# Optimization experiments

Measured on AMD Instinct MI355X. Metric: run time of the kernel, lower is better.

Reference implementation:

```python
import jax, jax.numpy as jnp
import numpy as np

N_NODES = 50000
N_EDGES = 800000
EMBED = 128
HEADS = 8
HEAD_DIM = EMBED // HEADS  # 16
HIDDEN = 512
EPS = 1e-5
SLOPE = 0.2  # DGL GATConv default negative_slope


def setup_inputs() -> dict:
    key = jax.random.key(0)
    ks = jax.random.split(key, 16)
    s = 0.05
    return {
        "x": jax.random.normal(ks[0], (N_NODES, EMBED), dtype=jnp.float32),
        "src": jax.random.randint(ks[1], (N_EDGES,), 0, N_NODES),
        "dst": jax.random.randint(ks[2], (N_EDGES,), 0, N_NODES),
        # GATConv params: fc weight stored as [in, out] (i.e. torch weight transposed)
        "W": jax.random.normal(ks[3], (EMBED, HEADS * HEAD_DIM), dtype=jnp.float32) * s,
        "attn_l": jax.random.normal(ks[4], (HEADS, HEAD_DIM), dtype=jnp.float32) * s,
        "attn_r": jax.random.normal(ks[5], (HEADS, HEAD_DIM), dtype=jnp.float32) * s,
        "gat_bias": jnp.zeros((EMBED,), dtype=jnp.float32),
        # BatchNorm1d affine params (training-mode batch stats used in math)
        "gamma1": jnp.ones((EMBED,), dtype=jnp.float32),
        "beta1": jnp.zeros((EMBED,), dtype=jnp.float32),
        "gamma2": jnp.ones((EMBED,), dtype=jnp.float32),
        "beta2": jnp.zeros((EMBED,), dtype=jnp.float32),
        # FFN weights stored as [in, out]
        "W1": jax.random.normal(ks[6], (EMBED, HIDDEN), dtype=jnp.float32) * s,
        "b1": jnp.zeros((HIDDEN,), dtype=jnp.float32),
        "W2": jax.random.normal(ks[7], (HIDDEN, EMBED), dtype=jnp.float32) * s,
        "b2": jnp.zeros((EMBED,), dtype=jnp.float32),
    }


def _batchnorm(y, gamma, beta):
    mu = jnp.mean(y, axis=0)
    var = jnp.var(y, axis=0)  # biased variance, as torch BN uses for normalization
    return gamma * (y - mu) * jax.lax.rsqrt(var + EPS) + beta


def reference(x, src, dst, W, attn_l, attn_r, gat_bias,
              gamma1, beta1, gamma2, beta2, W1, b1, W2, b2):
    N = x.shape[0]
    # ---- GATConv ----
    feat = (x @ W).reshape(N, HEADS, HEAD_DIM)              # [N,H,D]
    el = jnp.sum(feat * attn_l, axis=-1)                    # [N,H]
    er = jnp.sum(feat * attn_r, axis=-1)                    # [N,H]
    e = jax.nn.leaky_relu(el[src] + er[dst], SLOPE)         # [E,H]
    # segment softmax over incoming edges of each dst node
    m = jax.ops.segment_max(e, dst, num_segments=N)         # [N,H] (-inf for empty)
    ex = jnp.exp(e - m[dst])                                # [E,H]
    denom = jax.ops.segment_sum(ex, dst, num_segments=N)    # [N,H]
    a = ex / denom[dst]                                     # [E,H]
    msg = feat[src] * a[:, :, None]                         # [E,H,D]
    rst = jax.ops.segment_sum(msg, dst, num_segments=N)     # [N,H,D]
    rst = rst + gat_bias.reshape(HEADS, HEAD_DIM)
    h = x + rst.reshape(N, EMBED)                           # skip connection
    # ---- FFN block: BN -> skip(MLP) -> BN ----
    h = _batchnorm(h, gamma1, beta1)
    y = jax.nn.relu(h @ W1 + b1) @ W2 + b2
    h = _batchnorm(h + y, gamma2, beta2)
    return h
```

## Files before the change

kernel.cpp:

```cpp
#include <hip/hip_runtime.h>

#define NCH 128
#define NH  8
#define HID 512
#define SLOPE 0.2f
#define BN_EPS 1e-5f
#define LDP 136
#define NPW 4

typedef __attribute__((ext_vector_type(8))) short short8;
typedef __attribute__((ext_vector_type(4))) float floatx4;

__device__ inline unsigned short f2bf(float f) {
  unsigned u = __float_as_uint(f);
  u += 0x7fffu + ((u >> 16) & 1u);
  return (unsigned short)(u >> 16);
}
__device__ inline float bflo(unsigned u) { return __uint_as_float(u << 16); }
__device__ inline float bfhi(unsigned u) { return __uint_as_float(u & 0xffff0000u); }

__global__ void prep_all(const float* __restrict__ W, unsigned short* __restrict__ WT,
                         const float* __restrict__ W1, unsigned short* __restrict__ w1f,
                         const float* __restrict__ W2, unsigned short* __restrict__ w2f,
                         float* __restrict__ stats, int* __restrict__ cnt, int N) {
  int b = blockIdx.x, tid = threadIdx.x;
  if (b < 64) {
    int i = b * 256 + tid;
    int n = i >> 7, k = i & 127;
    WT[i] = f2bf(W[k * NCH + n]);
  } else if (b < 320) {
    int i = (b - 64) * 256 + tid;
    int ntile = i >> 11, kk = (i >> 9) & 3, lane = (i >> 3) & 63, j = i & 7;
    int k = kk * 32 + (lane >> 4) * 8 + j;
    int n = ntile * 16 + (lane & 15);
    w1f[i] = f2bf(W1[k * HID + n]);
  } else if (b < 576) {
    int i = (b - 320) * 256 + tid;
    int ch = i >> 14, nt = (i >> 11) & 7, kk = (i >> 9) & 3, lane = (i >> 3) & 63, j = i & 7;
    int k = ch * 128 + kk * 32 + (lane >> 4) * 8 + j;
    int n = nt * 16 + (lane & 15);
    w2f[i] = f2bf(W2[k * NCH + n]);
  } else if (b < 596) {
    int i = (b - 576) * 256 + tid;
    ((float4*)stats)[i] = make_float4(0.f, 0.f, 0.f, 0.f);
  } else {
    int i = (b - 596) * 256 + tid;
    int n4 = (N + 3) >> 2;
    if (i < n4) ((int4*)cnt)[i] = make_int4(0, 0, 0, 0);
  }
}

__global__ __launch_bounds__(256) void feat_mfma(const float* __restrict__ x,
                                                 const unsigned short* __restrict__ WT,
                                                 const float* __restrict__ attn_l,
                                                 const float* __restrict__ attn_r,
                                                 unsigned short* __restrict__ featb,
                                                 float* __restrict__ el, float* __restrict__ er,
                                                 int N) {
  __shared__ unsigned short rowX[64 * LDP];
  __shared__ unsigned short wt[128 * LDP];
  __shared__ float alr[256];
  int tid = threadIdx.x;
  int r0 = blockIdx.x * 64;
  int lane = tid & 63, wid = tid >> 6;
  int quad = lane >> 4, lc = lane & 15;
  int mrow = (wid & 1) * 32;
  int chalf = (wid >> 1) * 64;

  alr[tid] = (tid < 128) ? attn_l[tid] : attn_r[tid - 128];
  {
    int n = tid >> 1, kg = (tid & 1) * 64;
    const uint4* g = (const uint4*)(WT + n * NCH + kg);
    uint4* l = (uint4*)&wt[n * LDP + kg];
    for (int i = 0; i < 8; i++) l[i] = g[i];
  }
  {
    int r = tid >> 2, kg = (tid & 3) * 32;
    int gr = r0 + r;
    unsigned short tmp[32];
    if (gr < N) {
      const float4* gp = (const float4*)(x + (size_t)gr * NCH + kg);
      for (int i = 0; i < 8; i++) {
        float4 v = gp[i];
        tmp[i * 4 + 0] = f2bf(v.x); tmp[i * 4 + 1] = f2bf(v.y);
        tmp[i * 4 + 2] = f2bf(v.z); tmp[i * 4 + 3] = f2bf(v.w);
      }
    } else {
      for (int i = 0; i < 32; i++) tmp[i] = 0;
    }
    uint4* l = (uint4*)&rowX[r * LDP + kg];
    const uint4* s = (const uint4*)tmp;
    for (int i = 0; i < 4; i++) l[i] = s[i];
  }
  __syncthreads();

  floatx4 acc[2][4];
  for (int rt = 0; rt < 2; rt++) for (int tt = 0; tt < 4; tt++) acc[rt][tt] = (floatx4)(0.f);
  for (int kk = 0; kk < 4; kk++) {
    short8 a0 = *(const short8*)&rowX[(mrow + lc) * LDP + kk * 32 + quad * 8];
    short8 a1 = *(const short8*)&rowX[(mrow + 16 + lc) * LDP + kk * 32 + quad * 8];
    for (int tt = 0; tt < 4; tt++) {
      short8 b = *(const short8*)&wt[(chalf + tt * 16 + lc) * LDP + kk * 32 + quad * 8];
      acc[0][tt] = __builtin_amdgcn_mfma_f32_16x16x32_bf16(a0, b, acc[0][tt], 0, 0, 0);
      acc[1][tt] = __builtin_amdgcn_mfma_f32_16x16x32_bf16(a1, b, acc[1][tt], 0, 0, 0);
    }
  }
  __syncthreads();
  for (int rt = 0; rt < 2; rt++)
    for (int tt = 0; tt < 4; tt++)
      for (int r = 0; r < 4; r++)
        rowX[(mrow + rt * 16 + quad * 4 + r) * LDP + chalf + tt * 16 + lc] = f2bf(acc[rt][tt][r]);
  __syncthreads();
  {
    int r = tid >> 2, kg = (tid & 3) * 32;
    int gr = r0 + r;
    if (gr < N) {
      uint4* gp = (uint4*)(featb + (size_t)gr * NCH + kg);
      const uint4* l = (const uint4*)&rowX[r * LDP + kg];
      for (int i = 0; i < 4; i++) gp[i] = l[i];
    }
  }
  for (int p = tid; p < 512; p += 256) {
    int row = p >> 3, h = p & 7;
    int gr = r0 + row;
    if (gr < N) {
      const unsigned* rp = (const unsigned*)&rowX[row * LDP + h * 16];
      float sl = 0.f, sr = 0.f;
      for (int q = 0; q < 8; q++) {
        unsigned u = rp[q];
        float lo = bflo(u), hi = bfhi(u);
        int c = h * 16 + 2 * q;
        sl += lo * alr[c] + hi * alr[c + 1];
        sr += lo * alr[128 + c] + hi * alr[128 + c + 1];
      }
      el[gr * NH + h] = sl;
      er[gr * NH + h] = sr;
    }
  }
}

__global__ void edge_hist(const int* __restrict__ dst, int* __restrict__ cnt, int E) {
  int i = blockIdx.x * 256 + threadIdx.x;
  if (i < E) atomicAdd(&cnt[dst[i]], 1);
}

__global__ void scan_part(const int* __restrict__ cnt, int* __restrict__ off,
                          int* __restrict__ bsum, int N) {
  __shared__ int sh[256];
  int t = threadIdx.x, i = blockIdx.x * 256 + t;
  int v = (i < N) ? cnt[i] : 0;
  sh[t] = v; __syncthreads();
  for (int d = 1; d < 256; d <<= 1) {
    int u = (t >= d) ? sh[t - d] : 0;
    __syncthreads();
    sh[t] += u;
    __syncthreads();
  }
  if (i < N) off[i] = sh[t] - v;
  if (t == 255) bsum[blockIdx.x] = sh[255];
}

__global__ void scan_top(int* __restrict__ bsum, int nb) {
  __shared__ int sh[256];
  int t = threadIdx.x;
  int v = (t < nb) ? bsum[t] : 0;
  sh[t] = v; __syncthreads();
  for (int d = 1; d < 256; d <<= 1) {
    int u = (t >= d) ? sh[t - d] : 0;
    __syncthreads();
    sh[t] += u;
    __syncthreads();
  }
  if (t < nb) bsum[t] = sh[t] - v;
}

__global__ void scan_add(int* __restrict__ off, const int* __restrict__ bsum,
                         int* __restrict__ cursor, int N) {
  int i = blockIdx.x * 256 + threadIdx.x;
  if (i < N) {
    int v = off[i] + bsum[blockIdx.x];
    off[i] = v;
    cursor[i] = v;
  }
}

__global__ void edge_scatter(const int* __restrict__ src, const int* __restrict__ dst,
                             int* __restrict__ cursor, int* __restrict__ ssrc, int E) {
  int i = blockIdx.x * 256 + threadIdx.x;
  if (i < E) {
    int p = atomicAdd(&cursor[dst[i]], 1);
    ssrc[p] = src[i];
  }
}

__global__ __launch_bounds__(256) void gat_gather6(const int* __restrict__ ssrc,
                                                   const int* __restrict__ off,
                                                   const int* __restrict__ cnt,
                                                   const float* __restrict__ el,
                                                   const float* __restrict__ er,
                                                   const unsigned short* __restrict__ featb,
                                                   const float* __restrict__ x,
                                                   const float* __restrict__ gatb,
                                                   float* __restrict__ hbuf,
                                                   float* __restrict__ stats, int N) {
  __shared__ float ps[4][128], pq[4][128];
  int tid = threadIdx.x;
  int lane = tid & 63, w = tid >> 6;
  int hme = lane >> 3;
  int c0 = 2 * lane;
  float gb0 = gatb[c0], gb1 = gatb[c0 + 1];
  float s0 = 0.f, s1 = 0.f, q0 = 0.f, q1 = 0.f;
  int base = blockIdx.x * (4 * NPW) + w * NPW;
  for (int j = 0; j < NPW; j++) {
    int node = base + j;
    if (node >= N) break;
    node = __builtin_amdgcn_readfirstlane(node);
    float erh = er[node * NH + hme];
    int beg = __builtin_amdgcn_readfirstlane(off[node]);
    int num = __builtin_amdgcn_readfirstlane(cnt[node]);
    const int* sp = ssrc + beg;
    float acc0 = 0.f, acc1 = 0.f, den = 0.f;
    int i = 0;
    for (; i + 8 <= num; i += 8) {
      int n0 = __builtin_amdgcn_readfirstlane(sp[i + 0]);
      int n1 = __builtin_amdgcn_readfirstlane(sp[i + 1]);
      int n2 = __builtin_amdgcn_readfirstlane(sp[i + 2]);
      int n3 = __builtin_amdgcn_readfirstlane(sp[i + 3]);
      int n4 = __builtin_amdgcn_readfirstlane(sp[i + 4]);
      int n5 = __builtin_amdgcn_readfirstlane(sp[i + 5]);
      int n6 = __builtin_amdgcn_readfirstlane(sp[i + 6]);
      int n7 = __builtin_amdgcn_readfirstlane(sp[i + 7]);
      unsigned f0 = ((const unsigned*)(featb + (size_t)n0 * NCH))[lane];
      unsigned f1 = ((const unsigned*)(featb + (size_t)n1 * NCH))[lane];
      unsigned f2 = ((const unsigned*)(featb + (size_t)n2 * NCH))[lane];
      unsigned f3 = ((const unsigned*)(featb + (size_t)n3 * NCH))[lane];
      unsigned f4 = ((const unsigned*)(featb + (size_t)n4 * NCH))[lane];
      unsigned f5 = ((const unsigned*)(featb + (size_t)n5 * NCH))[lane];
      unsigned f6 = ((const unsigned*)(featb + (size_t)n6 * NCH))[lane];
      unsigned f7 = ((const unsigned*)(featb + (size_t)n7 * NCH))[lane];
      float e0 = el[n0 * NH + hme] + erh, e1 = el[n1 * NH + hme] + erh;
      float e2 = el[n2 * NH + hme] + erh, e3 = el[n3 * NH + hme] + erh;
      float e4 = el[n4 * NH + hme] + erh, e5 = el[n5 * NH + hme] + erh;
      float e6 = el[n6 * NH + hme] + erh, e7 = el[n7 * NH + hme] + erh;
      e0 = e0 > 0.f ? e0 : SLOPE * e0;  e1 = e1 > 0.f ? e1 : SLOPE * e1;
      e2 = e2 > 0.f ? e2 : SLOPE * e2;  e3 = e3 > 0.f ? e3 : SLOPE * e3;
      e4 = e4 > 0.f ? e4 : SLOPE * e4;  e5 = e5 > 0.f ? e5 : SLOPE * e5;
      e6 = e6 > 0.f ? e6 : SLOPE * e6;  e7 = e7 > 0.f ? e7 : SLOPE * e7;
      float w0 = __expf(e0), w1 = __expf(e1), w2 = __expf(e2), w3 = __expf(e3);
      float w4 = __expf(e4), w5 = __expf(e5), w6 = __expf(e6), w7 = __expf(e7);
      acc0 += w0 * bflo(f0) + w1 * bflo(f1) + w2 * bflo(f2) + w3 * bflo(f3)
            + w4 * bflo(f4) + w5 * bflo(f5) + w6 * bflo(f6) + w7 * bflo(f7);
      acc1 += w0 * bfhi(f0) + w1 * bfhi(f1) + w2 * bfhi(f2) + w3 * bfhi(f3)
            + w4 * bfhi(f4) + w5 * bfhi(f5) + w6 * bfhi(f6) + w7 * bfhi(f7);
      den  += w0 + w1 + w2 + w3 + w4 + w5 + w6 + w7;
    }
    for (; i + 4 <= num; i += 4) {
      int n0 = __builtin_amdgcn_readfirstlane(sp[i + 0]);
      int n1 = __builtin_amdgcn_readfirstlane(sp[i + 1]);
      int n2 = __builtin_amdgcn_readfirstlane(sp[i + 2]);
      int n3 = __builtin_amdgcn_readfirstlane(sp[i + 3]);
      unsigned f0 = ((const unsigned*)(featb + (size_t)n0 * NCH))[lane];
      unsigned f1 = ((const unsigned*)(featb + (size_t)n1 * NCH))[lane];
      unsigned f2 = ((const unsigned*)(featb + (size_t)n2 * NCH))[lane];
      unsigned f3 = ((const unsigned*)(featb + (size_t)n3 * NCH))[lane];
      float e0 = el[n0 * NH + hme] + erh, e1 = el[n1 * NH + hme] + erh;
      float e2 = el[n2 * NH + hme] + erh, e3 = el[n3 * NH + hme] + erh;
      e0 = e0 > 0.f ? e0 : SLOPE * e0;  e1 = e1 > 0.f ? e1 : SLOPE * e1;
      e2 = e2 > 0.f ? e2 : SLOPE * e2;  e3 = e3 > 0.f ? e3 : SLOPE * e3;
      float w0 = __expf(e0), w1 = __expf(e1), w2 = __expf(e2), w3 = __expf(e3);
      acc0 += w0 * bflo(f0) + w1 * bflo(f1) + w2 * bflo(f2) + w3 * bflo(f3);
      acc1 += w0 * bfhi(f0) + w1 * bfhi(f1) + w2 * bfhi(f2) + w3 * bfhi(f3);
      den  += w0 + w1 + w2 + w3;
    }
    for (; i < num; i++) {
      int s = __builtin_amdgcn_readfirstlane(sp[i]);
      unsigned f = ((const unsigned*)(featb + (size_t)s * NCH))[lane];
      float e = el[s * NH + hme] + erh;
      e = e > 0.f ? e : SLOPE * e;
      float wv = __expf(e);
      acc0 += wv * bflo(f); acc1 += wv * bfhi(f); den += wv;
    }
    float inv = den > 0.f ? 1.f / den : 0.f;
    float2 xv = *(const float2*)(x + (size_t)node * NCH + c0);
    float h0 = xv.x + acc0 * inv + gb0;
    float h1 = xv.y + acc1 * inv + gb1;
    *(float2*)(hbuf + (size_t)node * NCH + c0) = make_float2(h0, h1);
    s0 += h0; s1 += h1; q0 += h0 * h0; q1 += h1 * h1;
  }
  ps[w][c0] = s0; ps[w][c0 + 1] = s1;
  pq[w][c0] = q0; pq[w][c0 + 1] = q1;
  __syncthreads();
  if (tid < 128) {
    float ss = ps[0][tid] + ps[1][tid] + ps[2][tid] + ps[3][tid];
    float qq = pq[0][tid] + pq[1][tid] + pq[2][tid] + pq[3][tid];
    int rep = blockIdx.x & 3;
    atomicAdd(&stats[rep * 2048 + tid * 16], ss);
    atomicAdd(&stats[8192 + rep * 2048 + tid * 16], qq);
  }
}

__global__ void stats_finalize(const float* __restrict__ stats, float* __restrict__ mu,
                               float* __restrict__ rs, int n, int so_sum, int so_sq, int nrep) {
  int c = threadIdx.x;
  if (c < 128) {
    float s = 0.f, sq = 0.f;
    for (int r = 0; r < nrep; r++) {
      s  += stats[so_sum + r * 2048 + c * 16];
      sq += stats[so_sq  + r * 2048 + c * 16];
    }
    float m = s / (float)n;
    float v = sq / (float)n - m * m;
    mu[c] = m;
    rs[c] = rsqrtf(v + BN_EPS);
  }
}

__global__ __launch_bounds__(512, 4) void ffn_mfma2(const float* __restrict__ hbuf,
                                                    const float* __restrict__ mu1, const float* __restrict__ rs1,
                                                    const float* __restrict__ g1, const float* __restrict__ be1,
                                                    const unsigned short* __restrict__ w1f,
                                                    const unsigned short* __restrict__ w2f,
                                                    const float* __restrict__ b1, const float* __restrict__ b2,
                                                    float* __restrict__ t, float* __restrict__ stats, int N) {
  __shared__ unsigned short w1t[16384];
  __shared__ unsigned short w2t[16384];
  __shared__ unsigned short scr[8][512];
  __shared__ float b1L[512];
  __shared__ float psc[128], psh[128], b2L[128], csum[128], csq[128];
  int tid = threadIdx.x;
  int lane = tid & 63, wid = tid >> 6;
  int quad = lane >> 4, lc = lane & 15;
  int r0 = blockIdx.x * 128;

  b1L[tid] = b1[tid];
  if (tid < 128) {
    float s = g1[tid] * rs1[tid];
    psc[tid] = s;
    psh[tid] = be1[tid] - s * mu1[tid];
    b2L[tid] = b2[tid];
    csum[tid] = 0.f; csq[tid] = 0.f;
  }

  int arow = r0 + wid * 16 + lc;
  float4 av[4][2];
  for (int kk = 0; kk < 4; kk++) {
    if (arow < N) {
      const float4* p = (const float4*)(hbuf + (size_t)arow * NCH + kk * 32 + quad * 8);
      av[kk][0] = p[0]; av[kk][1] = p[1];
    } else {
      av[kk][0] = make_float4(0.f, 0.f, 0.f, 0.f);
      av[kk][1] = make_float4(0.f, 0.f, 0.f, 0.f);
    }
  }
  __syncthreads();

  short8 rowA[4];
  for (int kk = 0; kk < 4; kk++) {
    int c = kk * 32 + quad * 8;
    float4 s0 = *(float4*)&psc[c], s1 = *(float4*)&psc[c + 4];
    float4 h0 = *(float4*)&psh[c], h1 = *(float4*)&psh[c + 4];
    short8 r;
    r[0] = (short)f2bf(av[kk][0].x * s0.x + h0.x);
    r[1] = (short)f2bf(av[kk][0].y * s0.y + h0.y);
    r[2] = (short)f2bf(av[kk][0].z * s0.z + h0.z);
    r[3] = (short)f2bf(av[kk][0].w * s0.w + h0.w);
    r[4] = (short)f2bf(av[kk][1].x * s1.x + h1.x);
    r[5] = (short)f2bf(av[kk][1].y * s1.y + h1.y);
    r[6] = (short)f2bf(av[kk][1].z * s1.z + h1.z);
    r[7] = (short)f2bf(av[kk][1].w * s1.w + h1.w);
    rowA[kk] = r;
  }

  floatx4 acc2[8];
  for (int nt = 0; nt < 8; nt++) acc2[nt] = (floatx4)(0.f);

  for (int ch = 0; ch < 4; ch++) {
    __syncthreads();
    {
      const uint4* g1p = (const uint4*)(w1f + ch * 16384);
      const uint4* g2p = (const uint4*)(w2f + ch * 16384);
      uint4* l1 = (uint4*)w1t;
      uint4* l2 = (uint4*)w2t;
      for (int r = 0; r < 4; r++) {
        l1[tid + r * 512] = g1p[tid + r * 512];
        l2[tid + r * 512] = g2p[tid + r * 512];
      }
    }
    __syncthreads();

    for (int kk = 0; kk < 4; kk++) {
      floatx4 d0 = (floatx4)(0.f), d1 = (floatx4)(0.f);
      int t0 = 2 * kk, t1 = 2 * kk + 1;
      for (int kp = 0; kp < 4; kp++) {
        short8 a0 = *(const short8*)&w1t[(t0 * 4 + kp) * 512 + lane * 8];
        short8 a1 = *(const short8*)&w1t[(t1 * 4 + kp) * 512 + lane * 8];
        d0 = __builtin_amdgcn_mfma_f32_16x16x32_bf16(a0, rowA[kp], d0, 0, 0, 0);
        d1 = __builtin_amdgcn_mfma_f32_16x16x32_bf16(a1, rowA[kp], d1, 0, 0, 0);
      }
      {
        int bi0 = ch * 128 + t0 * 16 + 4 * quad;
        float4 bv0 = *(float4*)&b1L[bi0];
        float4 bv1 = *(float4*)&b1L[bi0 + 16];
        float v0, v1, v2, v3;
        unsigned lo, hi;
        int sidx;
        v0 = fmaxf(d0[0] + bv0.x, 0.f); v1 = fmaxf(d0[1] + bv0.y, 0.f);
        v2 = fmaxf(d0[2] + bv0.z, 0.f); v3 = fmaxf(d0[3] + bv0.w, 0.f);
        lo = (unsigned)f2bf(v0) | ((unsigned)f2bf(v1) << 16);
        hi = (unsigned)f2bf(v2) | ((unsigned)f2bf(v3) << 16);
        sidx = ((quad >> 1) * 16 + lc) * 8 + 4 * (quad & 1);
        *(uint2*)&scr[wid][sidx] = make_uint2(lo, hi);
        v0 = fmaxf(d1[0] + bv1.x, 0.f); v1 = fmaxf(d1[1] + bv1.y, 0.f);
        v2 = fmaxf(d1[2] + bv1.z, 0.f); v3 = fmaxf(d1[3] + bv1.w, 0.f);
        lo = (unsigned)f2bf(v0) | ((unsigned)f2bf(v1) << 16);
        hi = (unsigned)f2bf(v2) | ((unsigned)f2bf(v3) << 16);
        sidx = ((2 + (quad >> 1)) * 16 + lc) * 8 + 4 * (quad & 1);
        *(uint2*)&scr[wid][sidx] = make_uint2(lo, hi);
      }
      short8 a2 = *(const short8*)&scr[wid][lane * 8];
      for (int nt = 0; nt < 8; nt++) {
        short8 bfr = *(const short8*)&w2t[(nt * 4 + kk) * 512 + lane * 8];
        acc2[nt] = __builtin_amdgcn_mfma_f32_16x16x32_bf16(a2, bfr, acc2[nt], 0, 0, 0);
      }
    }
  }

  for (int nt = 0; nt < 8; nt++) {
    int col = nt * 16 + lc;
    float sc = psc[col], sh = psh[col], b2v = b2L[col];
    float s = 0.f, q = 0.f;
    for (int reg = 0; reg < 4; reg++) {
      int grow = r0 + wid * 16 + quad * 4 + reg;
      if (grow < N) {
        float hb = hbuf[(size_t)grow * NCH + col];
        float base = __uint_as_float(((unsigned)f2bf(sc * hb + sh)) << 16);
        float tv = base + acc2[nt][reg] + b2v;
        t[(size_t)grow * NCH + col] = tv;
        s += tv; q += tv * tv;
      }
    }
    s += __shfl_xor(s, 16); s += __shfl_xor(s, 32);
    q += __shfl_xor(q, 16); q += __shfl_xor(q, 32);
    if (quad == 0) { atomicAdd(&csum[col], s); atomicAdd(&csq[col], q); }
  }
  __syncthreads();
  if (tid < 128) {
    atomicAdd(&stats[16384 + tid * 16], csum[tid]);
    atomicAdd(&stats[18432 + tid * 16], csq[tid]);
  }
}

__global__ void bn2_apply(const float* __restrict__ t,
                          const float* __restrict__ g, const float* __restrict__ b,
                          const float* __restrict__ mu, const float* __restrict__ rs,
                          float* __restrict__ out, int total) {
  int i = blockIdx.x * blockDim.x + threadIdx.x;
  if (i >= total) return;
  int c = i & 127;
  out[i] = g[c] * (t[i] - mu[c]) * rs[c] + b[c];
}

extern "C" void kernel_launch(void* const* d_in, const int* in_sizes, int n_in,
                              void* d_out, int out_size, void* d_ws, size_t ws_size,
                              hipStream_t stream) {
  const float* x       = (const float*)d_in[0];
  const int*   src     = (const int*)d_in[1];
  const int*   dst     = (const int*)d_in[2];
  const float* W       = (const float*)d_in[3];
  const float* attn_l  = (const float*)d_in[4];
  const float* attn_r  = (const float*)d_in[5];
  const float* gatb    = (const float*)d_in[6];
  const float* gamma1  = (const float*)d_in[7];
  const float* beta1   = (const float*)d_in[8];
  const float* gamma2  = (const float*)d_in[9];
  const float* beta2   = (const float*)d_in[10];
  const float* W1      = (const float*)d_in[11];
  const float* b1      = (const float*)d_in[12];
  const float* W2      = (const float*)d_in[13];
  const float* b2      = (const float*)d_in[14];
  float* out = (float*)d_out;

  const int N = in_sizes[0] / NCH;
  const int E = in_sizes[1];
  const int nb = (N + 255) / 256;

  float* hbuf  = (float*)d_ws;
  float* t     = hbuf + (size_t)N * NCH;
  float* el    = t + (size_t)N * NCH;
  float* er    = el + (size_t)N * NH;
  float* stats = er + (size_t)N * NH;
  float* mus   = stats + 20480;
  unsigned short* featb = (unsigned short*)(mus + 512);
  unsigned short* WT    = featb + (size_t)N * NCH;
  unsigned short* w1f   = WT + NCH * NCH;
  unsigned short* w2f   = w1f + HID * NCH;
  int* cnt    = (int*)(w2f + HID * NCH);
  int* off    = cnt + N;
  int* cursor = off + N;
  int* bsum   = cursor + N;
  int* ssrc   = bsum + 256;

  const int cb = (((N + 3) / 4) + 255) / 256;
  prep_all<<<596 + cb, 256, 0, stream>>>(W, WT, W1, w1f, W2, w2f, stats, cnt, N);

  feat_mfma<<<(N + 63) / 64, 256, 0, stream>>>(x, WT, attn_l, attn_r, featb, el, er, N);

  edge_hist<<<(E + 255) / 256, 256, 0, stream>>>(dst, cnt, E);
  scan_part<<<nb, 256, 0, stream>>>(cnt, off, bsum, N);
  scan_top<<<1, 256, 0, stream>>>(bsum, nb);
  scan_add<<<nb, 256, 0, stream>>>(off, bsum, cursor, N);
  edge_scatter<<<(E + 255) / 256, 256, 0, stream>>>(src, dst, cursor, ssrc, E);

  gat_gather6<<<(N + 4 * NPW - 1) / (4 * NPW), 256, 0, stream>>>(ssrc, off, cnt, el, er, featb,
                                                                 x, gatb, hbuf, stats, N);
  stats_finalize<<<1, 128, 0, stream>>>(stats, mus, mus + 128, N, 0, 8192, 4);

  ffn_mfma2<<<(N + 127) / 128, 512, 0, stream>>>(hbuf, mus, mus + 128, gamma1, beta1,
                                                 w1f, w2f, b1, b2, t, stats, N);
  stats_finalize<<<1, 128, 0, stream>>>(stats, mus + 256, mus + 384, N, 16384, 18432, 1);

  bn2_apply<<<(N * NCH + 255) / 256, 256, 0, stream>>>(t, gamma2, beta2,
                                                       mus + 256, mus + 384, out, N * NCH);
}
```

Baseline: 324.6 us.

## Fuse launches: merge hist into feat kernel, fold scans and stats finalize into consumers

Merges the edge histogram into the feature MFMA kernel as extra blocks, merges the top-level scan into the scan-add kernel (each block recomputes the block prefix), and folds both BN stats finalizations into the FFN and BN2 apply kernels. BN2 apply is also vectorised to float4. This removes four kernel launches and their serialisation gaps, at the cost of redundant per-block stats and scan recomputation. The histogram atomics now run concurrently with the MFMA blocks.

```diff
diff --git a/kernel.cpp b/kernel.cpp
--- a/kernel.cpp
+++ b/kernel.cpp
@@ -50,16 +50,23 @@
   }
 }
 
-__global__ __launch_bounds__(256) void feat_mfma(const float* __restrict__ x,
+__global__ __launch_bounds__(256) void feat_hist(const float* __restrict__ x,
                                                  const unsigned short* __restrict__ WT,
                                                  const float* __restrict__ attn_l,
                                                  const float* __restrict__ attn_r,
                                                  unsigned short* __restrict__ featb,
                                                  float* __restrict__ el, float* __restrict__ er,
-                                                 int N) {
+                                                 int N,
+                                                 const int* __restrict__ dst, int* __restrict__ cnt,
+                                                 int E, int FB) {
   __shared__ unsigned short rowX[64 * LDP];
   __shared__ unsigned short wt[128 * LDP];
   __shared__ float alr[256];
+  if (blockIdx.x >= FB) {
+    int i = (blockIdx.x - FB) * 256 + threadIdx.x;
+    if (i < E) atomicAdd(&cnt[dst[i]], 1);
+    return;
+  }
   int tid = threadIdx.x;
   int r0 = blockIdx.x * 64;
   int lane = tid & 63, wid = tid >> 6;
@@ -139,11 +146,6 @@
   }
 }
 
-__global__ void edge_hist(const int* __restrict__ dst, int* __restrict__ cnt, int E) {
-  int i = blockIdx.x * 256 + threadIdx.x;
-  if (i < E) atomicAdd(&cnt[dst[i]], 1);
-}
-
 __global__ void scan_part(const int* __restrict__ cnt, int* __restrict__ off,
                           int* __restrict__ bsum, int N) {
   __shared__ int sh[256];
@@ -160,7 +162,8 @@
   if (t == 255) bsum[blockIdx.x] = sh[255];
 }
 
-__global__ void scan_top(int* __restrict__ bsum, int nb) {
+__global__ void scan_add2(int* __restrict__ off, const int* __restrict__ bsum,
+                          int* __restrict__ cursor, int N, int nb) {
   __shared__ int sh[256];
   int t = threadIdx.x;
   int v = (t < nb) ? bsum[t] : 0;
@@ -171,16 +174,12 @@
     sh[t] += u;
     __syncthreads();
   }
-  if (t < nb) bsum[t] = sh[t] - v;
-}
-
-__global__ void scan_add(int* __restrict__ off, const int* __restrict__ bsum,
-                         int* __restrict__ cursor, int N) {
-  int i = blockIdx.x * 256 + threadIdx.x;
+  int pref = (blockIdx.x > 0) ? sh[blockIdx.x - 1] : 0;
+  int i = blockIdx.x * 256 + t;
   if (i < N) {
-    int v = off[i] + bsum[blockIdx.x];
-    off[i] = v;
-    cursor[i] = v;
+    int w = off[i] + pref;
+    off[i] = w;
+    cursor[i] = w;
   }
 }
 
@@ -299,24 +298,7 @@
   }
 }
 
-__global__ void stats_finalize(const float* __restrict__ stats, float* __restrict__ mu,
-                               float* __restrict__ rs, int n, int so_sum, int so_sq, int nrep) {
-  int c = threadIdx.x;
-  if (c < 128) {
-    float s = 0.f, sq = 0.f;
-    for (int r = 0; r < nrep; r++) {
-      s  += stats[so_sum + r * 2048 + c * 16];
-      sq += stats[so_sq  + r * 2048 + c * 16];
-    }
-    float m = s / (float)n;
-    float v = sq / (float)n - m * m;
-    mu[c] = m;
-    rs[c] = rsqrtf(v + BN_EPS);
-  }
-}
-
 __global__ __launch_bounds__(512, 4) void ffn_mfma2(const float* __restrict__ hbuf,
-                                                    const float* __restrict__ mu1, const float* __restrict__ rs1,
                                                     const float* __restrict__ g1, const float* __restrict__ be1,
                                                     const unsigned short* __restrict__ w1f,
                                                     const unsigned short* __restrict__ w2f,
@@ -334,9 +316,17 @@
 
   b1L[tid] = b1[tid];
   if (tid < 128) {
-    float s = g1[tid] * rs1[tid];
-    psc[tid] = s;
-    psh[tid] = be1[tid] - s * mu1[tid];
+    float s = 0.f, sq = 0.f;
+    for (int r = 0; r < 4; r++) {
+      s  += stats[r * 2048 + tid * 16];
+      sq += stats[8192 + r * 2048 + tid * 16];
+    }
+    float m = s / (float)N;
+    float v = sq / (float)N - m * m;
+    float rsv = rsqrtf(v + BN_EPS);
+    float scv = g1[tid] * rsv;
+    psc[tid] = scv;
+    psh[tid] = be1[tid] - scv * m;
     b2L[tid] = b2[tid];
     csum[tid] = 0.f; csq[tid] = 0.f;
   }
@@ -450,14 +440,34 @@
   }
 }
 
-__global__ void bn2_apply(const float* __restrict__ t,
-                          const float* __restrict__ g, const float* __restrict__ b,
-                          const float* __restrict__ mu, const float* __restrict__ rs,
-                          float* __restrict__ out, int total) {
-  int i = blockIdx.x * blockDim.x + threadIdx.x;
-  if (i >= total) return;
-  int c = i & 127;
-  out[i] = g[c] * (t[i] - mu[c]) * rs[c] + b[c];
+__global__ __launch_bounds__(256) void bn2_apply2(const float* __restrict__ t,
+                                                  const float* __restrict__ g, const float* __restrict__ b,
+                                                  const float* __restrict__ stats,
+                                                  float* __restrict__ out, int N) {
+  __shared__ float scs[128], shs[128];
+  int tid = threadIdx.x;
+  if (tid < 128) {
+    float s = stats[16384 + tid * 16], sq = stats[18432 + tid * 16];
+    float m = s / (float)N;
+    float v = sq / (float)N - m * m;
+    float rsv = rsqrtf(v + BN_EPS);
+    float gg = g[tid] * rsv;
+    scs[tid] = gg;
+    shs[tid] = b[tid] - gg * m;
+  }
+  __syncthreads();
+  int i = blockIdx.x * 256 + tid;
+  int tot4 = N * 32;
+  if (i < tot4) {
+    float4 v = ((const float4*)t)[i];
+    int c = (i & 31) * 4;
+    float4 o;
+    o.x = v.x * scs[c + 0] + shs[c + 0];
+    o.y = v.y * scs[c + 1] + shs[c + 1];
+    o.z = v.z * scs[c + 2] + shs[c + 2];
+    o.w = v.w * scs[c + 3] + shs[c + 3];
+    ((float4*)out)[i] = o;
+  }
 }
 
 extern "C" void kernel_launch(void* const* d_in, const int* in_sizes, int n_in,
@@ -483,6 +493,8 @@
   const int N = in_sizes[0] / NCH;
   const int E = in_sizes[1];
   const int nb = (N + 255) / 256;
+  const int EB = (E + 255) / 256;
+  const int FB = (N + 63) / 64;
 
   float* hbuf  = (float*)d_ws;
   float* t     = hbuf + (size_t)N * NCH;
@@ -503,22 +515,18 @@
   const int cb = (((N + 3) / 4) + 255) / 256;
   prep_all<<<596 + cb, 256, 0, stream>>>(W, WT, W1, w1f, W2, w2f, stats, cnt, N);
 
-  feat_mfma<<<(N + 63) / 64, 256, 0, stream>>>(x, WT, attn_l, attn_r, featb, el, er, N);
-
-  edge_hist<<<(E + 255) / 256, 256, 0, stream>>>(dst, cnt, E);
+  feat_hist<<<FB + EB, 256, 0, stream>>>(x, WT, attn_l, attn_r, featb, el, er, N,
+                                         dst, cnt, E, FB);
+
   scan_part<<<nb, 256, 0, stream>>>(cnt, off, bsum, N);
-  scan_top<<<1, 256, 0, stream>>>(bsum, nb);
-  scan_add<<<nb, 256, 0, stream>>>(off, bsum, cursor, N);
-  edge_scatter<<<(E + 255) / 256, 256, 0, stream>>>(src, dst, cursor, ssrc, E);
+  scan_add2<<<nb, 256, 0, stream>>>(off, bsum, cursor, N, nb);
+  edge_scatter<<<EB, 256, 0, stream>>>(src, dst, cursor, ssrc, E);
 
   gat_gather6<<<(N + 4 * NPW - 1) / (4 * NPW), 256, 0, stream>>>(ssrc, off, cnt, el, er, featb,
                                                                  x, gatb, hbuf, stats, N);
-  stats_finalize<<<1, 128, 0, stream>>>(stats, mus, mus + 128, N, 0, 8192, 4);
-
-  ffn_mfma2<<<(N + 127) / 128, 512, 0, stream>>>(hbuf, mus, mus + 128, gamma1, beta1,
+
+  ffn_mfma2<<<(N + 127) / 128, 512, 0, stream>>>(hbuf, gamma1, beta1,
                                                  w1f, w2f, b1, b2, t, stats, N);
-  stats_finalize<<<1, 128, 0, stream>>>(stats, mus + 256, mus + 384, N, 16384, 18432, 1);
-
-  bn2_apply<<<(N * NCH + 255) / 256, 256, 0, stream>>>(t, gamma2, beta2,
-                                                       mus + 256, mus + 384, out, N * NCH);
-}
+
+  bn2_apply2<<<(N * 32 + 255) / 256, 256, 0, stream>>>(t, gamma2, beta2, stats, out, N);
+}
```

Result: faster. 317.9 us (-2.1%).
